# Performance work log

Hardware: AMD Instinct MI355X
Metric: run time of the kernel (lower is better)

Reference implementation:

```python
import jax, jax.numpy as jnp
import numpy as np

N, S, R, M, C, CZ = 1, 128, 256, 256, 32, 128


def setup_inputs() -> dict:
    key = jax.random.key(0)
    k1, k2, k3, k4 = jax.random.split(key, 4)
    return {
        "msa_repr": jax.random.normal(k1, (N, S, R, M), dtype=jnp.float32) * 0.1,
        "left_w": jax.random.normal(k2, (M, C), dtype=jnp.float32) * 0.02,
        "right_w": jax.random.normal(k3, (M, C), dtype=jnp.float32) * 0.02,
        "out_w": jax.random.normal(k4, (C * C, CZ), dtype=jnp.float32) * 0.02,
    }


def reference(msa_repr, left_w, right_w, out_w):
    # msa_repr: [N,S,R,M]
    n, s, r, m = msa_repr.shape
    c = left_w.shape[1]
    # opm_projection: [N,S,R,M] @ [M,C] -> [N,S,R,C]
    left = jnp.einsum('nsrm,mc->nsrc', msa_repr, left_w)
    right = jnp.einsum('nsrm,mc->nsrc', msa_repr, right_w)
    # outer product summed over MSA dim s: [N,R,T,C,C]
    # (torch: a=left.transpose(-2,-3) -> [N,R,S,C]; einsum '...bac,...dae->...bdce')
    outer = jnp.einsum('nsrc,nste->nrtce', left, right).reshape(n, r, r, c * c)
    # project to pair channel: [N,R,T,C*C] @ [C*C,CZ] -> [N,R,T,CZ]
    return jnp.matmul(outer, out_w)
```

## Files before the change

kernel.cpp:

```cpp
#include <hip/hip_runtime.h>
#include <stdint.h>

#define S_DIM 128
#define R_DIM 256
#define M_DIM 256
#define C_DIM 32
#define CZ_DIM 128
#define K2_DIM 1024

typedef _Float16 f16;
typedef _Float16 f16x4 __attribute__((ext_vector_type(4)));
typedef _Float16 f16x8 __attribute__((ext_vector_type(8)));
typedef float f32x4 __attribute__((ext_vector_type(4)));
typedef float f32x16 __attribute__((ext_vector_type(16)));

typedef const __attribute__((address_space(1))) uint32_t gu32_t;
typedef __attribute__((address_space(3))) uint32_t lu32_t;
#define GLOAD_LDS16(g, l) \
    __builtin_amdgcn_global_load_lds((gu32_t*)(g), (lu32_t*)(l), 16, 0, 0)

__global__ __launch_bounds__(256, 4)
void proj_kernel(const float* __restrict__ msa, const float* __restrict__ lw,
                 const float* __restrict__ rw, const float* __restrict__ ow,
                 f16* __restrict__ left_t, f16* __restrict__ rt2,
                 f16* __restrict__ wt2) {
    __shared__ __align__(16) f16 wlT[8192];
    __shared__ __align__(16) f16 wrT[8192];

    int bid = blockIdx.x;
    int tid = threadIdx.x;
    int w = tid >> 6;
    int lane = tid & 63;
    int q = lane >> 4, li = lane & 15;
    int r  = bid >> 1;
    int s0 = (bid & 1) << 6;
    int s_col = s0 + w * 16 + li;

    const f32x4* bp = (const f32x4*)(msa + ((size_t)s_col * R_DIM + r) * M_DIM + q * 8);
    f32x4 b[16];
#pragma unroll
    for (int ks = 0; ks < 8; ks++) { b[2 * ks] = bp[ks * 8]; b[2 * ks + 1] = bp[ks * 8 + 1]; }

    {
        int i = bid * 256 + tid;
        int cz = i >> 10, k2 = i & 1023;
        int c = k2 >> 5, e = k2 & 31;
        int k2p = ((e >> 2) << 7) + (c << 2) + (e & 3);
        int ntile = cz >> 5, l31o = cz & 31;
        int kk = k2p >> 4, q5o = (k2p >> 3) & 1, j = k2p & 7;
        wt2[(ntile * 64 + kk) * 512 + (l31o * 2 + q5o) * 8 + j] = (f16)ow[k2 * CZ_DIM + cz];
    }
#pragma unroll
    for (int k = 0; k < 32; k++) {
        int i = k * 256 + tid;
        int m = i >> 5, c = i & 31;
        int d = ((m >> 3) * 32 + c) * 8 + (m & 7);
        wlT[d] = (f16)lw[i];
        wrT[d] = (f16)rw[i];
    }
    __syncthreads();

    f32x4 aL0 = {0,0,0,0}, aL1 = {0,0,0,0}, aR0 = {0,0,0,0}, aR1 = {0,0,0,0};
#pragma unroll
    for (int ks = 0; ks < 8; ks++) {
        f16x8 bf;
#pragma unroll
        for (int u = 0; u < 4; u++) { bf[u] = (f16)b[2*ks][u]; bf[4 + u] = (f16)b[2*ks+1][u]; }
        const f16* a0 = wlT + ((ks * 4 + q) * 32 + li) * 8;
        const f16* a1 = wrT + ((ks * 4 + q) * 32 + li) * 8;
        f16x8 al0 = *(const f16x8*)(a0);
        f16x8 al1 = *(const f16x8*)(a0 + 128);
        f16x8 ar0 = *(const f16x8*)(a1);
        f16x8 ar1 = *(const f16x8*)(a1 + 128);
        aL0 = __builtin_amdgcn_mfma_f32_16x16x32_f16(al0, bf, aL0, 0, 0, 0);
        aL1 = __builtin_amdgcn_mfma_f32_16x16x32_f16(al1, bf, aL1, 0, 0, 0);
        aR0 = __builtin_amdgcn_mfma_f32_16x16x32_f16(ar0, bf, aR0, 0, 0, 0);
        aR1 = __builtin_amdgcn_mfma_f32_16x16x32_f16(ar1, bf, aR1, 0, 0, 0);
    }

    __syncthreads();
    f16* bL = wlT;
    f16* bR = wlT + 2048;
    {
        int sc7 = (s_col >> 3) & 7, sj = s_col & 7;
        int kl = (s_col >> 4) & 3;
        int q5_s = (s_col >> 3) & 1;
#pragma unroll
        for (int reg = 0; reg < 4; reg++) {
            int c0 = q * 4 + reg;
            int o = ((sc7 ^ c0) & 7) * 8 + sj;
            bL[c0 * 64 + o]        = (f16)aL0[reg];
            bL[(c0 + 16) * 64 + o] = (f16)aL1[reg];
            bR[kl * 512 + c0 * 16 + q5_s * 8 + sj]        = (f16)aR0[reg];
            bR[kl * 512 + (c0 + 16) * 16 + q5_s * 8 + sj] = (f16)aR1[reg];
        }
    }
    __syncthreads();

    {
        int sH = s0 >> 6;
        int lr = tid >> 3;
        int H = ((lr & 8) >> 3) ^ sH;
        f16* Lb = left_t + (size_t)(r >> 3) * 32768;
        *(f16x8*)(Lb + ((r & 7) * 32 + lr) * 128 + H * 64 + (tid & 7) * 8) =
            *(const f16x8*)(bL + lr * 64 + (tid & 7) * 8);

        int kl2 = tid >> 6, ix = tid & 63;
        *(f16x8*)(rt2 + (size_t)(r * 8 + (s0 >> 4) + kl2) * 512 + ix * 8) =
            *(const f16x8*)(bR + kl2 * 512 + ix * 8);
    }
}

__global__ __launch_bounds__(512, 4)
void fuse_kernel(const f16* __restrict__ left_t, const f16* __restrict__ rt2,
                 const f16* __restrict__ wt2, float* __restrict__ out) {
    __shared__ __align__(16) char lds[65536];
    f16* Ls = (f16*)lds;

    int bid0 = blockIdx.x;
    int bid = (bid0 & 7) * 256 + (bid0 >> 3);
    int br = bid >> 6, bt = bid & 63;
    int tid = threadIdx.x;
    int w = tid >> 6, lane = tid & 63;
    int q5 = lane >> 5, l31 = lane & 31, lx = lane & 15;

    const f16* Lg = left_t + (size_t)br * 32768;

#pragma unroll
    for (int it = 0; it < 8; it++) {
        GLOAD_LDS16(Lg + (size_t)(it * 512 + tid) * 8, Ls + (it * 512 + tid) * 8);
    }

    int t_tile = w & 3, rg4 = w >> 2;
    int g = bt * 4 + t_tile;
    const f16* ap = rt2 + (size_t)g * 4096 + (l31 * 2 + q5) * 8;
    f16x8 afr[8];
#pragma unroll
    for (int ks = 0; ks < 8; ks++) afr[ks] = *(const f16x8*)(ap + ks * 512);

    __syncthreads();

    f32x16 acc[4] = {};
    __builtin_amdgcn_s_setprio(1);
#pragma unroll
    for (int i = 0; i < 4; i++) {
        const f16* bbase = Ls + ((rg4 * 4 + i) * 32 + l31) * 128;
#pragma unroll
        for (int ks = 0; ks < 8; ks++) {
            f16x8 bfr = *(const f16x8*)(bbase + (((2 * ks + q5) ^ lx) << 3));
            acc[i] = __builtin_amdgcn_mfma_f32_32x32x16_f16(afr[ks], bfr, acc[i], 0, 0, 0);
        }
    }
    __builtin_amdgcn_s_setprio(0);

    int ntile = w & 3, kh = w >> 2;
    const f16* wbase = wt2 + (size_t)(ntile * 64 + kh * 32) * 512 + (l31 * 2 + q5) * 8;
    f16x8 wfg[8][4];
#pragma unroll
    for (int u = 0; u < 4; u++) wfg[0][u] = *(const f16x8*)(wbase + u * 512);

    __syncthreads();

    int chc = l31 >> 1, bsub = 8 * (l31 & 1);
#pragma unroll
    for (int i = 0; i < 4; i++) {
        int p = (rg4 * 4 + i) * 4 + t_tile;
        char* prow = lds + p * 2048;
#pragma unroll
        for (int rg = 0; rg < 4; rg++) {
            int ch = (2 * rg + q5) * 16 + chc;
            int phys = (ch + p) & 127;
            f16x4 h = {(f16)acc[i][4 * rg], (f16)acc[i][4 * rg + 1],
                       (f16)acc[i][4 * rg + 2], (f16)acc[i][4 * rg + 3]};
            *(f16x4*)(prow + phys * 16 + bsub) = h;
        }
    }
    __syncthreads();

    const char* lbase = lds + l31 * 2048;
    int base = 64 * kh + q5 + l31;
    f16x8 afg[8][4];
    f32x16 accA = {}, accB = {};
    __builtin_amdgcn_s_setprio(1);
#pragma unroll
    for (int gg = 0; gg < 8; gg++) {
        if (gg == 0) {
#pragma unroll
            for (int u = 0; u < 4; u++) wfg[1][u] = *(const f16x8*)(wbase + (4 + u) * 512);
#pragma unroll
            for (int u = 0; u < 4; u++) wfg[2][u] = *(const f16x8*)(wbase + (8 + u) * 512);
#pragma unroll
            for (int u = 0; u < 4; u++)
                afg[0][u] = *(const f16x8*)(lbase + (((base + 2 * u) & 127) << 4));
#pragma unroll
            for (int u = 0; u < 4; u++)
                afg[1][u] = *(const f16x8*)(lbase + (((base + 8 + 2 * u) & 127) << 4));
        } else {
            if (gg + 2 < 8) {
#pragma unroll
                for (int u = 0; u < 4; u++)
                    wfg[gg + 2][u] = *(const f16x8*)(wbase + ((gg + 2) * 4 + u) * 512);
            }
            if (gg + 1 < 8) {
#pragma unroll
                for (int u = 0; u < 4; u++)
                    afg[gg + 1][u] = *(const f16x8*)(lbase + (((base + (gg + 1) * 8 + 2 * u) & 127) << 4));
            }
        }
        accA = __builtin_amdgcn_mfma_f32_32x32x16_f16(afg[gg][0], wfg[gg][0], accA, 0, 0, 0);
        accB = __builtin_amdgcn_mfma_f32_32x32x16_f16(afg[gg][1], wfg[gg][1], accB, 0, 0, 0);
        accA = __builtin_amdgcn_mfma_f32_32x32x16_f16(afg[gg][2], wfg[gg][2], accA, 0, 0, 0);
        accB = __builtin_amdgcn_mfma_f32_32x32x16_f16(afg[gg][3], wfg[gg][3], accB, 0, 0, 0);
    }
    __builtin_amdgcn_s_setprio(0);
    f32x16 acc2;
#pragma unroll
    for (int v = 0; v < 16; v++) acc2[v] = accA[v] + accB[v];
    __syncthreads();

    if (w >= 4) {
        char* rb = lds + (w - 4) * 4096 + lane * 64;
#pragma unroll
        for (int u = 0; u < 4; u++) {
            f32x4 part = {acc2[4 * u], acc2[4 * u + 1], acc2[4 * u + 2], acc2[4 * u + 3]};
            *(f32x4*)(rb + u * 16) = part;
        }
    }
    __syncthreads();
    if (w < 4) {
        const char* rb = lds + w * 4096 + lane * 64;
#pragma unroll
        for (int u = 0; u < 4; u++) {
            f32x4 part = *(const f32x4*)(rb + u * 16);
#pragma unroll
            for (int v = 0; v < 4; v++) acc2[4 * u + v] += part[v];
        }
        int r0 = br * 8, t0 = bt * 4, cz = w * 32 + l31;
#pragma unroll
        for (int reg = 0; reg < 16; reg++) {
            int p = (reg & 3) + 8 * (reg >> 2) + 4 * q5;
            out[((size_t)((r0 + (p >> 2)) * R_DIM + t0 + (p & 3))) * CZ_DIM + cz] = acc2[reg];
        }
    }
}

extern "C" void kernel_launch(void* const* d_in, const int* in_sizes, int n_in,
                              void* d_out, int out_size, void* d_ws, size_t ws_size,
                              hipStream_t stream) {
    const float* msa = (const float*)d_in[0];
    const float* lw  = (const float*)d_in[1];
    const float* rw  = (const float*)d_in[2];
    const float* ow  = (const float*)d_in[3];
    char* ws = (char*)d_ws;
    f16* left_t = (f16*)(ws);
    f16* rt2    = (f16*)(ws + (size_t)2 * 1024 * 1024);
    f16* wt2    = (f16*)(ws + (size_t)4 * 1024 * 1024);
    float* out  = (float*)d_out;

    proj_kernel<<<dim3(512), dim3(256), 0, stream>>>(msa, lw, rw, ow, left_t, rt2, wt2);
    fuse_kernel<<<dim3(2048), dim3(512), 0, stream>>>(left_t, rt2, wt2, out);
}
```

Before: 134.0 us.

## Merge projection and fused outer-product kernels into one persistent dataflow kernel

Replaces the two kernel launches with a single kernel. Blocks take work items in order from an atomic counter: the first 256 items compute projections, one r row and 512 threads each, and the rest do the outer-product/projection tiles. Each fuse block spin-waits on per-row flags and a weight-ready counter before it starts, so fuse work can overlap with projection tails and one launch boundary is removed. In exchange it adds a memset launch, atomic polling and fences, and risks stalls if dependencies complete late.

```diff
diff --git a/kernel.cpp b/kernel.cpp
--- a/kernel.cpp
+++ b/kernel.cpp
@@ -7,6 +7,8 @@
 #define C_DIM 32
 #define CZ_DIM 128
 #define K2_DIM 1024
+#define NPROJ 256
+#define NFUSE 2048
 
 typedef _Float16 f16;
 typedef _Float16 f16x4 __attribute__((ext_vector_type(4)));
@@ -19,111 +21,132 @@
 #define GLOAD_LDS16(g, l) \
     __builtin_amdgcn_global_load_lds((gu32_t*)(g), (lu32_t*)(l), 16, 0, 0)
 
-__global__ __launch_bounds__(256, 4)
-void proj_kernel(const float* __restrict__ msa, const float* __restrict__ lw,
+__global__ __launch_bounds__(512, 4)
+void mega_kernel(const float* __restrict__ msa, const float* __restrict__ lw,
                  const float* __restrict__ rw, const float* __restrict__ ow,
                  f16* __restrict__ left_t, f16* __restrict__ rt2,
-                 f16* __restrict__ wt2) {
-    __shared__ __align__(16) f16 wlT[8192];
-    __shared__ __align__(16) f16 wrT[8192];
-
-    int bid = blockIdx.x;
+                 f16* __restrict__ wt2, float* __restrict__ out,
+                 unsigned* __restrict__ ctrl) {
+    __shared__ __align__(16) char lds[65536];
+    __shared__ int s_item;
+
+    unsigned* wctr = ctrl + 1;
+    unsigned* flag = ctrl + 2;
+
     int tid = threadIdx.x;
-    int w = tid >> 6;
-    int lane = tid & 63;
-    int q = lane >> 4, li = lane & 15;
-    int r  = bid >> 1;
-    int s0 = (bid & 1) << 6;
-    int s_col = s0 + w * 16 + li;
-
-    const f32x4* bp = (const f32x4*)(msa + ((size_t)s_col * R_DIM + r) * M_DIM + q * 8);
-    f32x4 b[16];
-#pragma unroll
-    for (int ks = 0; ks < 8; ks++) { b[2 * ks] = bp[ks * 8]; b[2 * ks + 1] = bp[ks * 8 + 1]; }
-
-    {
-        int i = bid * 256 + tid;
-        int cz = i >> 10, k2 = i & 1023;
-        int c = k2 >> 5, e = k2 & 31;
-        int k2p = ((e >> 2) << 7) + (c << 2) + (e & 3);
-        int ntile = cz >> 5, l31o = cz & 31;
-        int kk = k2p >> 4, q5o = (k2p >> 3) & 1, j = k2p & 7;
-        wt2[(ntile * 64 + kk) * 512 + (l31o * 2 + q5o) * 8 + j] = (f16)ow[k2 * CZ_DIM + cz];
-    }
-#pragma unroll
-    for (int k = 0; k < 32; k++) {
-        int i = k * 256 + tid;
-        int m = i >> 5, c = i & 31;
-        int d = ((m >> 3) * 32 + c) * 8 + (m & 7);
-        wlT[d] = (f16)lw[i];
-        wrT[d] = (f16)rw[i];
-    }
-    __syncthreads();
-
-    f32x4 aL0 = {0,0,0,0}, aL1 = {0,0,0,0}, aR0 = {0,0,0,0}, aR1 = {0,0,0,0};
-#pragma unroll
-    for (int ks = 0; ks < 8; ks++) {
-        f16x8 bf;
-#pragma unroll
-        for (int u = 0; u < 4; u++) { bf[u] = (f16)b[2*ks][u]; bf[4 + u] = (f16)b[2*ks+1][u]; }
-        const f16* a0 = wlT + ((ks * 4 + q) * 32 + li) * 8;
-        const f16* a1 = wrT + ((ks * 4 + q) * 32 + li) * 8;
-        f16x8 al0 = *(const f16x8*)(a0);
-        f16x8 al1 = *(const f16x8*)(a0 + 128);
-        f16x8 ar0 = *(const f16x8*)(a1);
-        f16x8 ar1 = *(const f16x8*)(a1 + 128);
-        aL0 = __builtin_amdgcn_mfma_f32_16x16x32_f16(al0, bf, aL0, 0, 0, 0);
-        aL1 = __builtin_amdgcn_mfma_f32_16x16x32_f16(al1, bf, aL1, 0, 0, 0);
-        aR0 = __builtin_amdgcn_mfma_f32_16x16x32_f16(ar0, bf, aR0, 0, 0, 0);
-        aR1 = __builtin_amdgcn_mfma_f32_16x16x32_f16(ar1, bf, aR1, 0, 0, 0);
-    }
-
-    __syncthreads();
-    f16* bL = wlT;
-    f16* bR = wlT + 2048;
-    {
-        int sc7 = (s_col >> 3) & 7, sj = s_col & 7;
-        int kl = (s_col >> 4) & 3;
-        int q5_s = (s_col >> 3) & 1;
-#pragma unroll
-        for (int reg = 0; reg < 4; reg++) {
-            int c0 = q * 4 + reg;
-            int o = ((sc7 ^ c0) & 7) * 8 + sj;
-            bL[c0 * 64 + o]        = (f16)aL0[reg];
-            bL[(c0 + 16) * 64 + o] = (f16)aL1[reg];
-            bR[kl * 512 + c0 * 16 + q5_s * 8 + sj]        = (f16)aR0[reg];
-            bR[kl * 512 + (c0 + 16) * 16 + q5_s * 8 + sj] = (f16)aR1[reg];
-        }
-    }
-    __syncthreads();
-
-    {
-        int sH = s0 >> 6;
-        int lr = tid >> 3;
-        int H = ((lr & 8) >> 3) ^ sH;
-        f16* Lb = left_t + (size_t)(r >> 3) * 32768;
-        *(f16x8*)(Lb + ((r & 7) * 32 + lr) * 128 + H * 64 + (tid & 7) * 8) =
-            *(const f16x8*)(bL + lr * 64 + (tid & 7) * 8);
-
-        int kl2 = tid >> 6, ix = tid & 63;
-        *(f16x8*)(rt2 + (size_t)(r * 8 + (s0 >> 4) + kl2) * 512 + ix * 8) =
-            *(const f16x8*)(bR + kl2 * 512 + ix * 8);
-    }
-}
-
-__global__ __launch_bounds__(512, 4)
-void fuse_kernel(const f16* __restrict__ left_t, const f16* __restrict__ rt2,
-                 const f16* __restrict__ wt2, float* __restrict__ out) {
-    __shared__ __align__(16) char lds[65536];
-    f16* Ls = (f16*)lds;
-
-    int bid0 = blockIdx.x;
-    int bid = (bid0 & 7) * 256 + (bid0 >> 3);
+    if (tid == 0) s_item = (int)atomicAdd(ctrl, 1u);
+    __syncthreads();
+    int item = s_item;
+
+    if (item < NPROJ) {
+        f16* wlT = (f16*)lds;
+        f16* wrT = (f16*)(lds + 16384);
+        int w = tid >> 6, lane = tid & 63;
+        int q = lane >> 4, li = lane & 15;
+        int r = item;
+        int sH = w >> 2;
+        int s_col = sH * 64 + (w & 3) * 16 + li;
+
+        const f32x4* bp = (const f32x4*)(msa + ((size_t)s_col * R_DIM + r) * M_DIM + q * 8);
+        f32x4 b[16];
+#pragma unroll
+        for (int ks = 0; ks < 8; ks++) { b[2*ks] = bp[ks*8]; b[2*ks+1] = bp[ks*8+1]; }
+
+        {
+            int i = item * 512 + tid;
+            int cz = i >> 10, k2 = i & 1023;
+            int c = k2 >> 5, e = k2 & 31;
+            int k2p = ((e >> 2) << 7) + (c << 2) + (e & 3);
+            int ntile = cz >> 5, l31o = cz & 31;
+            int kk = k2p >> 4, q5o = (k2p >> 3) & 1, j = k2p & 7;
+            wt2[(ntile * 64 + kk) * 512 + (l31o * 2 + q5o) * 8 + j] = (f16)ow[k2 * CZ_DIM + cz];
+        }
+        __threadfence();
+        __syncthreads();
+        if (tid == 0) atomicAdd(wctr, 1u);
+
+#pragma unroll
+        for (int k = 0; k < 16; k++) {
+            int i = k * 512 + tid;
+            int m = i >> 5, c = i & 31;
+            int d = ((m >> 3) * 32 + c) * 8 + (m & 7);
+            wlT[d] = (f16)lw[i];
+            wrT[d] = (f16)rw[i];
+        }
+        __syncthreads();
+
+        f32x4 aL0 = {0,0,0,0}, aL1 = {0,0,0,0}, aR0 = {0,0,0,0}, aR1 = {0,0,0,0};
+#pragma unroll
+        for (int ks = 0; ks < 8; ks++) {
+            f16x8 bf;
+#pragma unroll
+            for (int u = 0; u < 4; u++) { bf[u] = (f16)b[2*ks][u]; bf[4+u] = (f16)b[2*ks+1][u]; }
+            const f16* a0 = wlT + ((ks * 4 + q) * 32 + li) * 8;
+            const f16* a1 = wrT + ((ks * 4 + q) * 32 + li) * 8;
+            f16x8 al0 = *(const f16x8*)(a0);
+            f16x8 al1 = *(const f16x8*)(a0 + 128);
+            f16x8 ar0 = *(const f16x8*)(a1);
+            f16x8 ar1 = *(const f16x8*)(a1 + 128);
+            aL0 = __builtin_amdgcn_mfma_f32_16x16x32_f16(al0, bf, aL0, 0, 0, 0);
+            aL1 = __builtin_amdgcn_mfma_f32_16x16x32_f16(al1, bf, aL1, 0, 0, 0);
+            aR0 = __builtin_amdgcn_mfma_f32_16x16x32_f16(ar0, bf, aR0, 0, 0, 0);
+            aR1 = __builtin_amdgcn_mfma_f32_16x16x32_f16(ar1, bf, aR1, 0, 0, 0);
+        }
+
+        __syncthreads();
+        f16* bL = wlT;
+        f16* bR = wlT + 4096;
+        {
+            int sc7 = (s_col >> 3) & 7, sj = s_col & 7;
+            int klg = s_col >> 4;
+            int q5_s = (s_col >> 3) & 1;
+#pragma unroll
+            for (int reg = 0; reg < 4; reg++) {
+                int c0 = q * 4 + reg;
+                int o = ((sc7 ^ c0) & 7) * 8 + sj;
+                int H = ((c0 & 8) >> 3) ^ sH;
+                bL[c0 * 128 + H * 64 + o]        = (f16)aL0[reg];
+                bL[(c0 + 16) * 128 + H * 64 + o] = (f16)aL1[reg];
+                bR[klg * 512 + c0 * 16 + q5_s * 8 + sj]        = (f16)aR0[reg];
+                bR[klg * 512 + (c0 + 16) * 16 + q5_s * 8 + sj] = (f16)aR1[reg];
+            }
+        }
+        __syncthreads();
+
+        {
+            f16* Lb = left_t + (size_t)(r >> 3) * 32768;
+            int row = tid >> 4, col8 = tid & 15;
+            *(f16x8*)(Lb + ((r & 7) * 32 + row) * 128 + col8 * 8) =
+                *(const f16x8*)(bL + row * 128 + col8 * 8);
+            int ck = tid >> 6, ix = tid & 63;
+            *(f16x8*)(rt2 + (size_t)(r * 8 + ck) * 512 + ix * 8) =
+                *(const f16x8*)(bR + ck * 512 + ix * 8);
+        }
+        __threadfence();
+        __syncthreads();
+        if (tid == 0) atomicAdd(&flag[r], 1u);
+        return;
+    }
+
+    int it2 = item - NPROJ;
+    int bid = (it2 & 7) * 256 + (it2 >> 3);
     int br = bid >> 6, bt = bid & 63;
-    int tid = threadIdx.x;
     int w = tid >> 6, lane = tid & 63;
     int q5 = lane >> 5, l31 = lane & 31, lx = lane & 15;
 
+    if (tid == 0) {
+        while (atomicAdd(wctr, 0u) < NPROJ) __builtin_amdgcn_s_sleep(2);
+#pragma unroll 1
+        for (int k = 0; k < 8; k++)
+            while (atomicAdd(&flag[br * 8 + k], 0u) == 0u) __builtin_amdgcn_s_sleep(2);
+#pragma unroll 1
+        for (int k = 0; k < 4; k++)
+            while (atomicAdd(&flag[bt * 4 + k], 0u) == 0u) __builtin_amdgcn_s_sleep(2);
+        __threadfence();
+    }
+    __syncthreads();
+
+    f16* Ls = (f16*)lds;
     const f16* Lg = left_t + (size_t)br * 32768;
 
 #pragma unroll
@@ -153,8 +176,8 @@
     }
     __builtin_amdgcn_s_setprio(0);
 
-    int ntile = w & 3, kh = w >> 2;
-    const f16* wbase = wt2 + (size_t)(ntile * 64 + kh * 32) * 512 + (l31 * 2 + q5) * 8;
+    int kh = w >> 2;
+    const f16* wbase = wt2 + (size_t)(t_tile * 64 + kh * 32) * 512 + (l31 * 2 + q5) * 8;
     f16x8 wfg[8][4];
 #pragma unroll
     for (int u = 0; u < 4; u++) wfg[0][u] = *(const f16x8*)(wbase + u * 512);
@@ -255,8 +278,10 @@
     f16* left_t = (f16*)(ws);
     f16* rt2    = (f16*)(ws + (size_t)2 * 1024 * 1024);
     f16* wt2    = (f16*)(ws + (size_t)4 * 1024 * 1024);
+    unsigned* ctrl = (unsigned*)(ws + (size_t)4 * 1024 * 1024 + 262144);
     float* out  = (float*)d_out;
 
-    proj_kernel<<<dim3(512), dim3(256), 0, stream>>>(msa, lw, rw, ow, left_t, rt2, wt2);
-    fuse_kernel<<<dim3(2048), dim3(512), 0, stream>>>(left_t, rt2, wt2, out);
+    hipMemsetAsync(ctrl, 0, 4096, stream);
+    mega_kernel<<<dim3(NPROJ + NFUSE), dim3(512), 0, stream>>>(
+        msa, lw, rw, ow, left_t, rt2, wt2, out, ctrl);
 }
```

After: 442.7 us. 230% more time.
